# Kernel optimization log

Measured on AMD Instinct MI355X. Metric: run time of the kernel, lower is better.

## Reference

```python
import jax, jax.numpy as jnp
import numpy as np

B, S, D, H = 2, 2048, 1024, 16
HD = D // H


def setup_inputs() -> dict:
    key = jax.random.key(0)
    ks = jax.random.split(key, 12)
    s = 0.02
    inp = {
        "query": jax.random.normal(ks[0], (B, S, D), dtype=jnp.float32),
        "Wq": jax.random.normal(ks[1], (D, D), dtype=jnp.float32) * s,
        "bq": jnp.zeros((D,), jnp.float32),
        "Wk": jax.random.normal(ks[2], (D, D), dtype=jnp.float32) * s,
        "bk": jnp.zeros((D,), jnp.float32),
        "Wv": jax.random.normal(ks[3], (D, D), dtype=jnp.float32) * s,
        "bv": jnp.zeros((D,), jnp.float32),
        "Wo": jax.random.normal(ks[4], (D, D), dtype=jnp.float32) * s,
        "bo": jnp.zeros((D,), jnp.float32),
        "Wm1": jax.random.normal(ks[5], (D // 4, D), dtype=jnp.float32) * s,
        "bm1": jnp.zeros((D // 4,), jnp.float32),
        "Wm2": jax.random.normal(ks[6], (D, D // 4), dtype=jnp.float32) * s,
        "bm2": jnp.zeros((D,), jnp.float32),
        "dopamine": jnp.ones((1,), jnp.float32),
        "serotonin": jnp.ones((1,), jnp.float32),
        "norepinephrine": jnp.ones((1,), jnp.float32),
        "acetylcholine": jnp.ones((1,), jnp.float32),
        "attention_scale": jnp.ones((1,), jnp.float32),
        "attention_bias": jnp.zeros((1,), jnp.float32),
    }
    return inp


def reference(query, Wq, bq, Wk, bk, Wv, bv, Wo, bo, Wm1, bm1, Wm2, bm2,
              dopamine, serotonin, norepinephrine, acetylcholine,
              attention_scale, attention_bias):
    b, s, d = query.shape
    scale = HD ** -0.5
    split = lambda t: t.reshape(b, s, H, HD).transpose(0, 2, 1, 3)  # [b,h,s,hd]
    q = split(query @ Wq.T + bq)
    k = split(query @ Wk.T + bk)
    v = split(query @ Wv.T + bv)
    scores = jnp.einsum('bhqd,bhkd->bhqk', q, k) * scale
    w = jax.nn.softmax(scores, axis=-1)  # dropout=0 (eval)
    attn = jnp.einsum('bhqk,bhkd->bhqd', w, v)
    # neuromodulation MLP on flattened query, then combined scalar gate
    mod = jax.nn.relu(query @ Wm1.T + bm1) @ Wm2.T + bm2  # [b,s,d]
    gate = (dopamine + serotonin + norepinephrine + acetylcholine) / 4.0  # [1]
    neuro = split(mod * gate)  # [b,h,s,hd]
    attn = (attn * attention_scale + attention_bias) * (1.0 + neuro)
    out = attn.transpose(0, 2, 1, 3).reshape(b, s, d) @ Wo.T + bo
    return out
```

## Files before the change

### kernel.cpp

```cpp
#include <hip/hip_runtime.h>
#include <stdint.h>
#include <math.h>


typedef __attribute__((ext_vector_type(8))) short short8;
typedef __attribute__((ext_vector_type(8))) unsigned short ushort8;
typedef __attribute__((ext_vector_type(4))) float floatx4;

#define MFMA16(a, b, c) __builtin_amdgcn_mfma_f32_16x16x32_bf16(a, b, c, 0, 0, 0)

__device__ __forceinline__ unsigned short f2bf(float f) {
    union { float f; uint32_t u; } v; v.f = f;
    uint32_t r = v.u + 0x7fffu + ((v.u >> 16) & 1u);
    return (unsigned short)(r >> 16);
}
__device__ __forceinline__ float bf2f(unsigned short s) {
    union { uint32_t u; float f; } v; v.u = ((uint32_t)s) << 16;
    return v.f;
}

typedef const __attribute__((address_space(1))) void gvoid_t;
typedef __attribute__((address_space(3))) void lvoid_t;
__device__ __forceinline__ void gld16(const void* g, void* l) {
    __builtin_amdgcn_global_load_lds((gvoid_t*)g, (lvoid_t*)l, 16, 0, 0);
}

template<int BN, bool OUTBF>
__device__ __forceinline__ void gemm_core(const unsigned short* __restrict__ A,
                                          const unsigned short* __restrict__ W,
                                          const float* __restrict__ bias,
                                          void* __restrict__ C,
                                          int N, int K, int bm, int bn,
                                          bool relu, float osc)
{
    constexpr int MT = (BN == 128) ? 4 : 2;
    constexpr int SU = (BN == 128) ? 4 : 3;
    __shared__ __align__(16) unsigned short As[128][32];
    __shared__ __align__(16) unsigned short Ws[BN][32];

    const int tid  = threadIdx.x;
    const int w    = tid >> 6, lane = tid & 63;
    const int ln   = lane & 15, quad = lane >> 4;
    const int wm   = (BN == 128) ? (w >> 1) * 64 : w * 32;
    const int wn   = (BN == 128) ? (w & 1) * 64 : 0;

    floatx4 acc[MT][4] = {};

    for (int k0 = 0; k0 < K; k0 += 32) {
        __syncthreads();
        #pragma unroll
        for (int i = 0; i < SU; i++) {
            const int t = w * SU + i;
            if (t < 8) {
                const int r0  = t * 16;
                const int row = r0 + (lane >> 2);
                const int c   = (lane & 3) ^ ((row >> 1) & 3);
                gld16(&A[(size_t)(bm + row) * K + k0 + c * 8], &As[r0][0]);
            } else {
                const int r0  = (t - 8) * 16;
                const int row = r0 + (lane >> 2);
                const int c   = (lane & 3) ^ ((row >> 1) & 3);
                gld16(&W[(size_t)(bn + row) * K + k0 + c * 8], &Ws[r0][0]);
            }
        }
        __syncthreads();

        short8 af[MT], bf[4];
        #pragma unroll
        for (int mt = 0; mt < MT; mt++) {
            const int row = wm + mt * 16 + ln;
            af[mt] = *(const short8*)&As[row][(quad ^ ((row >> 1) & 3)) * 8];
        }
        #pragma unroll
        for (int nt = 0; nt < 4; nt++) {
            const int row = wn + nt * 16 + ln;
            bf[nt] = *(const short8*)&Ws[row][(quad ^ ((row >> 1) & 3)) * 8];
        }
        #pragma unroll
        for (int mt = 0; mt < MT; mt++)
            #pragma unroll
            for (int nt = 0; nt < 4; nt++)
                acc[mt][nt] = MFMA16(af[mt], bf[nt], acc[mt][nt]);
    }

    float bv[4];
    #pragma unroll
    for (int nt = 0; nt < 4; nt++) bv[nt] = bias[bn + wn + nt * 16 + ln];

    #pragma unroll
    for (int mt = 0; mt < MT; mt++) {
        #pragma unroll
        for (int nt = 0; nt < 4; nt++) {
            #pragma unroll
            for (int r = 0; r < 4; r++) {
                float v = (acc[mt][nt][r] + bv[nt]) * osc;
                if (relu) v = fmaxf(v, 0.f);
                const size_t row = (size_t)bm + wm + mt * 16 + quad * 4 + r;
                const size_t col = (size_t)bn + wn + nt * 16 + ln;
                if (OUTBF) ((unsigned short*)C)[row * N + col] = f2bf(v);
                else       ((float*)C)[row * N + col] = v;
            }
        }
    }
}

__global__ __launch_bounds__(256) void qkv_mlp1_gemm(
    const unsigned short* __restrict__ A,
    const unsigned short* __restrict__ Wq, const unsigned short* __restrict__ Wk,
    const unsigned short* __restrict__ Wv, const unsigned short* __restrict__ Wm1,
    const float* __restrict__ bq, const float* __restrict__ bk,
    const float* __restrict__ bv, const float* __restrict__ bm1,
    unsigned short* __restrict__ Qo, unsigned short* __restrict__ Ko,
    unsigned short* __restrict__ Vo, unsigned short* __restrict__ Ho)
{
    const int bx = blockIdx.x, bm = blockIdx.y * 128;
    const unsigned short* W; const float* bias; unsigned short* C;
    int N, bn; bool relu = false; float osc = 1.f;
    if (bx < 8)       { W = Wq;  bias = bq;  C = Qo; N = 1024; bn = bx * 128; osc = 0.125f; }
    else if (bx < 16) { W = Wk;  bias = bk;  C = Ko; N = 1024; bn = (bx - 8) * 128; }
    else if (bx < 24) { W = Wv;  bias = bv;  C = Vo; N = 1024; bn = (bx - 16) * 128; }
    else              { W = Wm1; bias = bm1; C = Ho; N = 256;  bn = (bx - 24) * 128; relu = true; }
    gemm_core<128, true>(A, W, bias, C, N, 1024, bm, bn, relu, osc);
}

template<bool OUTBF>
__global__ __launch_bounds__(256) void gemm_bn64(const unsigned short* __restrict__ A,
                                                 const unsigned short* __restrict__ W,
                                                 const float* __restrict__ bias,
                                                 void* __restrict__ C, int N, int K)
{
    gemm_core<64, OUTBF>(A, W, bias, C, N, K, blockIdx.y * 128, blockIdx.x * 64,
                         false, 1.f);
}

__global__ __launch_bounds__(256) void attn_mfma(const unsigned short* __restrict__ Qg,
                                                 const unsigned short* __restrict__ Kg,
                                                 const unsigned short* __restrict__ Vtg,
                                                 const unsigned short* __restrict__ Modg,
                                                 unsigned short* __restrict__ Yg,
                                                 const float* __restrict__ dop,
                                                 const float* __restrict__ ser,
                                                 const float* __restrict__ nor,
                                                 const float* __restrict__ ach,
                                                 const float* __restrict__ asc,
                                                 const float* __restrict__ abi)
{
    __shared__ __align__(16) unsigned short Ks[128][64];
    __shared__ __align__(16) unsigned short Vs[64][128];
    __shared__ __align__(16) unsigned short Ps[4][2][16][64];

    const int tid = threadIdx.x;
    const int w   = tid >> 6, lane = tid & 63;
    const int ln  = lane & 15, quad = lane >> 4;
    const int qt  = blockIdx.x, h = blockIdx.y, b = blockIdx.z;

    const size_t qrowbase = (size_t)b * 2048 + qt * 128 + w * 32;
    short8 qf[2][2];
    #pragma unroll
    for (int q2 = 0; q2 < 2; q2++) {
        const unsigned short* qp = Qg + (qrowbase + q2 * 16 + ln) * 1024 + h * 64;
        qf[q2][0] = *(const short8*)&qp[quad * 8];
        qf[q2][1] = *(const short8*)&qp[32 + quad * 8];
    }

    const size_t kbase = (size_t)b * 2048 * 1024 + h * 64;
    const size_t vbase = (size_t)(b * 16 + h) * 64 * 2048;

    floatx4 o[2][4] = {};
    float lsum[2] = {0.f, 0.f};

    for (int kc = 0; kc < 16; kc++) {
        __syncthreads();
        #pragma unroll
        for (int i = 0; i < 8; i++) {
            const int t = w * 8 + i;
            if (t < 16) {
                const int R = t * 8 + (lane >> 3);
                const int c = (lane & 7) ^ (R & 7);
                gld16(&Kg[kbase + (size_t)(kc * 128 + R) * 1024 + c * 8], &Ks[t * 8][0]);
            } else {
                const int tv = t - 16;
                const int R  = tv * 4 + (lane >> 4);
                const int c  = (lane & 15) ^ (R & 15);
                gld16(&Vtg[vbase + (size_t)R * 2048 + kc * 128 + c * 8], &Vs[tv * 4][0]);
            }
        }
        __syncthreads();

        #pragma unroll
        for (int half = 0; half < 2; half++) {
            #pragma unroll
            for (int q2 = 0; q2 < 2; q2++) {
                floatx4 sc[4];
                #pragma unroll
                for (int mt = 0; mt < 4; mt++) {
                    const int row = half * 64 + mt * 16 + ln;
                    const short8 kf0 = *(const short8*)&Ks[row][((0 + quad) ^ (ln & 7)) * 8];
                    const short8 kf1 = *(const short8*)&Ks[row][((4 + quad) ^ (ln & 7)) * 8];
                    floatx4 z = {};
                    z = MFMA16(kf0, qf[q2][0], z);
                    z = MFMA16(kf1, qf[q2][1], z);
                    sc[mt] = z;
                }
                #pragma unroll
                for (int mt = 0; mt < 4; mt++) {
                    const float p0 = __expf(sc[mt][0]);
                    const float p1 = __expf(sc[mt][1]);
                    const float p2 = __expf(sc[mt][2]);
                    const float p3 = __expf(sc[mt][3]);
                    lsum[q2] += (p0 + p1) + (p2 + p3);
                    uint2 pk;
                    pk.x = (uint32_t)f2bf(p0) | ((uint32_t)f2bf(p1) << 16);
                    pk.y = (uint32_t)f2bf(p2) | ((uint32_t)f2bf(p3) << 16);
                    const int c2 = (mt * 2 + (quad >> 1)) ^ (ln & 7);
                    *(uint2*)((char*)&Ps[w][q2][ln][0] + c2 * 16 + (quad & 1) * 8) = pk;
                }
            }

            short8 pf[2][2];
            #pragma unroll
            for (int q2 = 0; q2 < 2; q2++)
                #pragma unroll
                for (int ks = 0; ks < 2; ks++) {
                    const int c2 = (ks * 4 + quad) ^ (ln & 7);
                    pf[q2][ks] = *(const short8*)((char*)&Ps[w][q2][ln][0] + c2 * 16);
                }
            #pragma unroll
            for (int ntv = 0; ntv < 4; ntv++) {
                const int vrow = ntv * 16 + ln;
                #pragma unroll
                for (int ks = 0; ks < 2; ks++) {
                    const int c2 = (half * 8 + ks * 4 + quad) ^ (ln & 15);
                    const short8 vf = *(const short8*)&Vs[vrow][c2 * 8];
                    o[0][ntv] = MFMA16(pf[0][ks], vf, o[0][ntv]);
                    o[1][ntv] = MFMA16(pf[1][ks], vf, o[1][ntv]);
                }
            }
        }
    }

    #pragma unroll
    for (int q2 = 0; q2 < 2; q2++) {
        float s = lsum[q2];
        s += __shfl_xor(s, 16);
        s += __shfl_xor(s, 32);
        lsum[q2] = s;
    }

    const float gate = 0.25f * (dop[0] + ser[0] + nor[0] + ach[0]);
    const float scb = asc[0], bib = abi[0];
    #pragma unroll
    for (int q2 = 0; q2 < 2; q2++) {
        #pragma unroll
        for (int r = 0; r < 4; r++) {
            const float inv = 1.f / __shfl(lsum[q2], quad * 4 + r);
            const size_t row = qrowbase + q2 * 16 + quad * 4 + r;
            #pragma unroll
            for (int ntv = 0; ntv < 4; ntv++) {
                const size_t col = (size_t)h * 64 + ntv * 16 + ln;
                const float x  = o[q2][ntv][r] * inv;
                const float mo = bf2f(Modg[row * 1024 + col]);
                const float y  = (x * scb + bib) * (1.f + mo * gate);
                Yg[row * 1024 + col] = f2bf(y);
            }
        }
    }
}

__global__ __launch_bounds__(256) void transpose_v(const unsigned short* __restrict__ Vb,
                                                   unsigned short* __restrict__ Vt)
{
    __shared__ __align__(16) unsigned short T[64][72];
    const int tid = threadIdx.x;
    const int s0 = blockIdx.x * 64, h = blockIdx.y, b = blockIdx.z;
    const int g = tid & 7;
    #pragma unroll
    for (int p = 0; p < 2; p++) {
        const int row = p * 32 + (tid >> 3);
        const ushort8 v = *(const ushort8*)&Vb[(size_t)(b * 2048 + s0 + row) * 1024 + h * 64 + g * 8];
        *(ushort8*)&T[row][g * 8] = v;
    }
    __syncthreads();
    #pragma unroll
    for (int p = 0; p < 2; p++) {
        const int hd = p * 32 + (tid >> 3);
        ushort8 ov;
        #pragma unroll
        for (int j = 0; j < 8; j++) ov[j] = T[g * 8 + j][hd];
        *(ushort8*)&Vt[((size_t)(b * 16 + h) * 64 + hd) * 2048 + s0 + g * 8] = ov;
    }
}

__global__ __launch_bounds__(256) void fused_cast(
    const float* __restrict__ q,   const float* __restrict__ wq,
    const float* __restrict__ wk,  const float* __restrict__ wv,
    const float* __restrict__ wo,  const float* __restrict__ wm1,
    const float* __restrict__ wm2,
    unsigned short* __restrict__ dq,  unsigned short* __restrict__ dwq,
    unsigned short* __restrict__ dwk, unsigned short* __restrict__ dwv,
    unsigned short* __restrict__ dwo, unsigned short* __restrict__ dwm1,
    unsigned short* __restrict__ dwm2)
{
    const size_t u = (size_t)blockIdx.x * 256 + threadIdx.x;
    const float* src; unsigned short* dst; size_t off;
    if      (u <  524288) { src = q;   dst = dq;   off = u; }
    else if (u <  655360) { src = wq;  dst = dwq;  off = u - 524288; }
    else if (u <  786432) { src = wk;  dst = dwk;  off = u - 655360; }
    else if (u <  917504) { src = wv;  dst = dwv;  off = u - 786432; }
    else if (u < 1048576) { src = wo;  dst = dwo;  off = u - 917504; }
    else if (u < 1081344) { src = wm1; dst = dwm1; off = u - 1048576; }
    else                  { src = wm2; dst = dwm2; off = u - 1081344; }
    const float4* p = (const float4*)src + off * 2;
    const float4 a = p[0], c = p[1];
    ushort8 o;
    o[0] = f2bf(a.x); o[1] = f2bf(a.y); o[2] = f2bf(a.z); o[3] = f2bf(a.w);
    o[4] = f2bf(c.x); o[5] = f2bf(c.y); o[6] = f2bf(c.z); o[7] = f2bf(c.w);
    *(ushort8*)&dst[off * 8] = o;
}

extern "C" void kernel_launch(void* const* d_in, const int* in_sizes, int n_in,
                              void* d_out, int out_size, void* d_ws, size_t ws_size,
                              hipStream_t stream)
{
    const float* query = (const float*)d_in[0];
    const float* Wq  = (const float*)d_in[1];
    const float* bq  = (const float*)d_in[2];
    const float* Wk  = (const float*)d_in[3];
    const float* bk  = (const float*)d_in[4];
    const float* Wv  = (const float*)d_in[5];
    const float* bv  = (const float*)d_in[6];
    const float* Wo  = (const float*)d_in[7];
    const float* bo  = (const float*)d_in[8];
    const float* Wm1 = (const float*)d_in[9];
    const float* bm1 = (const float*)d_in[10];
    const float* Wm2 = (const float*)d_in[11];
    const float* bm2 = (const float*)d_in[12];
    const float* dop = (const float*)d_in[13];
    const float* ser = (const float*)d_in[14];
    const float* nor = (const float*)d_in[15];
    const float* ach = (const float*)d_in[16];
    const float* asc = (const float*)d_in[17];
    const float* abi = (const float*)d_in[18];

    char* ws = (char*)d_ws;
    const size_t MB = 1024 * 1024;
    unsigned short* Qry  = (unsigned short*)(ws);
    unsigned short* Wqb  = (unsigned short*)(ws + 8 * MB);
    unsigned short* Wkb  = (unsigned short*)(ws + 10 * MB);
    unsigned short* Wvb  = (unsigned short*)(ws + 12 * MB);
    unsigned short* Wob  = (unsigned short*)(ws + 14 * MB);
    unsigned short* Wm1b = (unsigned short*)(ws + 16 * MB);
    unsigned short* Wm2b = (unsigned short*)(ws + 16 * MB + 512 * 1024);
    unsigned short* Qb   = (unsigned short*)(ws + 17 * MB);
    unsigned short* Kb   = (unsigned short*)(ws + 25 * MB);
    unsigned short* Vb   = (unsigned short*)(ws + 33 * MB);
    unsigned short* Vt   = (unsigned short*)(ws + 41 * MB);
    unsigned short* Yb   = (unsigned short*)(ws + 49 * MB);
    unsigned short* Hm   = (unsigned short*)(ws + 57 * MB);
    unsigned short* Modb = Vb;

    fused_cast<<<4352, 256, 0, stream>>>(query, Wq, Wk, Wv, Wo, Wm1, Wm2,
                                         Qry, Wqb, Wkb, Wvb, Wob, Wm1b, Wm2b);

    qkv_mlp1_gemm<<<dim3(26, 32), 256, 0, stream>>>(
        Qry, Wqb, Wkb, Wvb, Wm1b, bq, bk, bv, bm1, Qb, Kb, Vb, Hm);

    transpose_v<<<dim3(32, 16, 2), 256, 0, stream>>>(Vb, Vt);

    gemm_bn64<true><<<dim3(16, 32), 256, 0, stream>>>(Hm, Wm2b, bm2, (void*)Modb, 1024, 256);

    attn_mfma<<<dim3(16, 16, 2), 256, 0, stream>>>(Qb, Kb, Vt, Modb, Yb,
                                                   dop, ser, nor, ach, asc, abi);

    gemm_bn64<false><<<dim3(16, 32), 256, 0, stream>>>(Yb, Wob, bo, d_out, 1024, 1024);
}
```

Baseline: 255.5 us.

## Fuse V transpose into QKV GEMM epilogue and double-buffer attention K/V tiles

```diff
diff --git a/kernel.cpp b/kernel.cpp
--- a/kernel.cpp
+++ b/kernel.cpp
@@ -1,4 +1,5 @@
 #include <hip/hip_runtime.h>
+#include <hip/hip_bf16.h>
 #include <stdint.h>
 #include <math.h>
 
@@ -17,6 +18,10 @@
 __device__ __forceinline__ float bf2f(unsigned short s) {
     union { uint32_t u; float f; } v; v.u = ((uint32_t)s) << 16;
     return v.f;
+}
+__device__ __forceinline__ uint32_t pk2(float a, float b) {
+    __hip_bfloat162 t = __float22bfloat162_rn(make_float2(a, b));
+    uint32_t u; __builtin_memcpy(&u, &t, 4); return u;
 }
 
 typedef const __attribute__((address_space(1))) void gvoid_t;
@@ -31,7 +36,8 @@
                                           const float* __restrict__ bias,
                                           void* __restrict__ C,
                                           int N, int K, int bm, int bn,
-                                          bool relu, float osc)
+                                          bool relu, float osc,
+                                          unsigned short* __restrict__ vt)
 {
     constexpr int MT = (BN == 128) ? 4 : 2;
     constexpr int SU = (BN == 128) ? 4 : 3;
@@ -87,6 +93,26 @@
     #pragma unroll
     for (int nt = 0; nt < 4; nt++) bv[nt] = bias[bn + wn + nt * 16 + ln];
 
+    if (vt != nullptr) {
+        #pragma unroll
+        for (int mt = 0; mt < MT; mt++) {
+            const int rowg = bm + wm + mt * 16 + quad * 4;
+            const int b = rowg >> 11, s = rowg & 2047;
+            #pragma unroll
+            for (int nt = 0; nt < 4; nt++) {
+                const int n = bn + wn + nt * 16 + ln;
+                const int h = n >> 6, hd = n & 63;
+                float v0 = acc[mt][nt][0] + bv[nt];
+                float v1 = acc[mt][nt][1] + bv[nt];
+                float v2 = acc[mt][nt][2] + bv[nt];
+                float v3 = acc[mt][nt][3] + bv[nt];
+                uint2 pk; pk.x = pk2(v0, v1); pk.y = pk2(v2, v3);
+                *(uint2*)&vt[((size_t)(b * 16 + h) * 64 + hd) * 2048 + s] = pk;
+            }
+        }
+        return;
+    }
+
     #pragma unroll
     for (int mt = 0; mt < MT; mt++) {
         #pragma unroll
@@ -111,16 +137,17 @@
     const float* __restrict__ bq, const float* __restrict__ bk,
     const float* __restrict__ bv, const float* __restrict__ bm1,
     unsigned short* __restrict__ Qo, unsigned short* __restrict__ Ko,
-    unsigned short* __restrict__ Vo, unsigned short* __restrict__ Ho)
+    unsigned short* __restrict__ Vt, unsigned short* __restrict__ Ho)
 {
     const int bx = blockIdx.x, bm = blockIdx.y * 128;
-    const unsigned short* W; const float* bias; unsigned short* C;
+    const unsigned short* W; const float* bias; unsigned short* C = nullptr;
+    unsigned short* vt = nullptr;
     int N, bn; bool relu = false; float osc = 1.f;
     if (bx < 8)       { W = Wq;  bias = bq;  C = Qo; N = 1024; bn = bx * 128; osc = 0.125f; }
     else if (bx < 16) { W = Wk;  bias = bk;  C = Ko; N = 1024; bn = (bx - 8) * 128; }
-    else if (bx < 24) { W = Wv;  bias = bv;  C = Vo; N = 1024; bn = (bx - 16) * 128; }
+    else if (bx < 24) { W = Wv;  bias = bv;  vt = Vt; N = 1024; bn = (bx - 16) * 128; }
     else              { W = Wm1; bias = bm1; C = Ho; N = 256;  bn = (bx - 24) * 128; relu = true; }
-    gemm_core<128, true>(A, W, bias, C, N, 1024, bm, bn, relu, osc);
+    gemm_core<128, true>(A, W, bias, C, N, 1024, bm, bn, relu, osc, vt);
 }
 
 template<bool OUTBF>
@@ -130,7 +157,7 @@
                                                  void* __restrict__ C, int N, int K)
 {
     gemm_core<64, OUTBF>(A, W, bias, C, N, K, blockIdx.y * 128, blockIdx.x * 64,
-                         false, 1.f);
+                         false, 1.f, nullptr);
 }
 
 __global__ __launch_bounds__(256) void attn_mfma(const unsigned short* __restrict__ Qg,
@@ -145,8 +172,8 @@
                                                  const float* __restrict__ asc,
                                                  const float* __restrict__ abi)
 {
-    __shared__ __align__(16) unsigned short Ks[128][64];
-    __shared__ __align__(16) unsigned short Vs[64][128];
+    __shared__ __align__(16) unsigned short Ks[2][128][64];
+    __shared__ __align__(16) unsigned short Vs[2][64][128];
     __shared__ __align__(16) unsigned short Ps[4][2][16][64];
 
     const int tid = threadIdx.x;
@@ -154,6 +181,9 @@
     const int ln  = lane & 15, quad = lane >> 4;
     const int qt  = blockIdx.x, h = blockIdx.y, b = blockIdx.z;
 
+    const size_t kbase = (size_t)b * 2048 * 1024 + h * 64;
+    const size_t vbase = (size_t)(b * 16 + h) * 64 * 2048;
+
     const size_t qrowbase = (size_t)b * 2048 + qt * 128 + w * 32;
     short8 qf[2][2];
     #pragma unroll
@@ -163,43 +193,51 @@
         qf[q2][1] = *(const short8*)&qp[32 + quad * 8];
     }
 
-    const size_t kbase = (size_t)b * 2048 * 1024 + h * 64;
-    const size_t vbase = (size_t)(b * 16 + h) * 64 * 2048;
-
     floatx4 o[2][4] = {};
     float lsum[2] = {0.f, 0.f};
 
-    for (int kc = 0; kc < 16; kc++) {
-        __syncthreads();
+    auto stage = [&](int kc, int bb) {
         #pragma unroll
         for (int i = 0; i < 8; i++) {
             const int t = w * 8 + i;
             if (t < 16) {
                 const int R = t * 8 + (lane >> 3);
                 const int c = (lane & 7) ^ (R & 7);
-                gld16(&Kg[kbase + (size_t)(kc * 128 + R) * 1024 + c * 8], &Ks[t * 8][0]);
+                gld16(&Kg[kbase + (size_t)(kc * 128 + R) * 1024 + c * 8], &Ks[bb][t * 8][0]);
             } else {
                 const int tv = t - 16;
                 const int R  = tv * 4 + (lane >> 4);
                 const int c  = (lane & 15) ^ (R & 15);
-                gld16(&Vtg[vbase + (size_t)R * 2048 + kc * 128 + c * 8], &Vs[tv * 4][0]);
-            }
-        }
+                gld16(&Vtg[vbase + (size_t)R * 2048 + kc * 128 + c * 8], &Vs[bb][tv * 4][0]);
+            }
+        }
+    };
+
+    stage(0, 0);
+
+    for (int kc = 0; kc < 16; kc++) {
+        const int bb = kc & 1;
         __syncthreads();
+        if (kc + 1 < 16) stage(kc + 1, bb ^ 1);
 
         #pragma unroll
         for (int half = 0; half < 2; half++) {
+            short8 kf[4][2];
+            #pragma unroll
+            for (int mt = 0; mt < 4; mt++) {
+                const int row = half * 64 + mt * 16 + ln;
+                kf[mt][0] = *(const short8*)&Ks[bb][row][((0 + quad) ^ (ln & 7)) * 8];
+                kf[mt][1] = *(const short8*)&Ks[bb][row][((4 + quad) ^ (ln & 7)) * 8];
+            }
+
             #pragma unroll
             for (int q2 = 0; q2 < 2; q2++) {
                 floatx4 sc[4];
                 #pragma unroll
                 for (int mt = 0; mt < 4; mt++) {
-                    const int row = half * 64 + mt * 16 + ln;
-                    const short8 kf0 = *(const short8*)&Ks[row][((0 + quad) ^ (ln & 7)) * 8];
-                    const short8 kf1 = *(const short8*)&Ks[row][((4 + quad) ^ (ln & 7)) * 8];
                     floatx4 z = {};
-                    z = MFMA16(kf0, qf[q2][0], z);
-                    z = MFMA16(kf1, qf[q2][1], z);
+                    z = MFMA16(kf[mt][0], qf[q2][0], z);
+                    z = MFMA16(kf[mt][1], qf[q2][1], z);
                     sc[mt] = z;
                 }
                 #pragma unroll
@@ -209,9 +247,7 @@
                     const float p2 = __expf(sc[mt][2]);
                     const float p3 = __expf(sc[mt][3]);
                     lsum[q2] += (p0 + p1) + (p2 + p3);
-                    uint2 pk;
-                    pk.x = (uint32_t)f2bf(p0) | ((uint32_t)f2bf(p1) << 16);
-                    pk.y = (uint32_t)f2bf(p2) | ((uint32_t)f2bf(p3) << 16);
+                    uint2 pk; pk.x = pk2(p0, p1); pk.y = pk2(p2, p3);
                     const int c2 = (mt * 2 + (quad >> 1)) ^ (ln & 7);
                     *(uint2*)((char*)&Ps[w][q2][ln][0] + c2 * 16 + (quad & 1) * 8) = pk;
                 }
@@ -231,7 +267,7 @@
                 #pragma unroll
                 for (int ks = 0; ks < 2; ks++) {
                     const int c2 = (half * 8 + ks * 4 + quad) ^ (ln & 15);
-                    const short8 vf = *(const short8*)&Vs[vrow][c2 * 8];
+                    const short8 vf = *(const short8*)&Vs[bb][vrow][c2 * 8];
                     o[0][ntv] = MFMA16(pf[0][ks], vf, o[0][ntv]);
                     o[1][ntv] = MFMA16(pf[1][ks], vf, o[1][ntv]);
                 }
@@ -264,30 +300,6 @@
                 Yg[row * 1024 + col] = f2bf(y);
             }
         }
-    }
-}
-
-__global__ __launch_bounds__(256) void transpose_v(const unsigned short* __restrict__ Vb,
-                                                   unsigned short* __restrict__ Vt)
-{
-    __shared__ __align__(16) unsigned short T[64][72];
-    const int tid = threadIdx.x;
-    const int s0 = blockIdx.x * 64, h = blockIdx.y, b = blockIdx.z;
-    const int g = tid & 7;
-    #pragma unroll
-    for (int p = 0; p < 2; p++) {
-        const int row = p * 32 + (tid >> 3);
-        const ushort8 v = *(const ushort8*)&Vb[(size_t)(b * 2048 + s0 + row) * 1024 + h * 64 + g * 8];
-        *(ushort8*)&T[row][g * 8] = v;
-    }
-    __syncthreads();
-    #pragma unroll
-    for (int p = 0; p < 2; p++) {
-        const int hd = p * 32 + (tid >> 3);
-        ushort8 ov;
-        #pragma unroll
-        for (int j = 0; j < 8; j++) ov[j] = T[g * 8 + j][hd];
-        *(ushort8*)&Vt[((size_t)(b * 16 + h) * 64 + hd) * 2048 + s0 + g * 8] = ov;
     }
 }
 
@@ -312,10 +324,10 @@
     else                  { src = wm2; dst = dwm2; off = u - 1081344; }
     const float4* p = (const float4*)src + off * 2;
     const float4 a = p[0], c = p[1];
-    ushort8 o;
-    o[0] = f2bf(a.x); o[1] = f2bf(a.y); o[2] = f2bf(a.z); o[3] = f2bf(a.w);
-    o[4] = f2bf(c.x); o[5] = f2bf(c.y); o[6] = f2bf(c.z); o[7] = f2bf(c.w);
-    *(ushort8*)&dst[off * 8] = o;
+    uint4 o;
+    o.x = pk2(a.x, a.y); o.y = pk2(a.z, a.w);
+    o.z = pk2(c.x, c.y); o.w = pk2(c.z, c.w);
+    *(uint4*)&dst[off * 8] = o;
 }
 
 extern "C" void kernel_launch(void* const* d_in, const int* in_sizes, int n_in,
@@ -353,19 +365,16 @@
     unsigned short* Wm2b = (unsigned short*)(ws + 16 * MB + 512 * 1024);
     unsigned short* Qb   = (unsigned short*)(ws + 17 * MB);
     unsigned short* Kb   = (unsigned short*)(ws + 25 * MB);
-    unsigned short* Vb   = (unsigned short*)(ws + 33 * MB);
+    unsigned short* Modb = (unsigned short*)(ws + 33 * MB);
     unsigned short* Vt   = (unsigned short*)(ws + 41 * MB);
     unsigned short* Yb   = (unsigned short*)(ws + 49 * MB);
     unsigned short* Hm   = (unsigned short*)(ws + 57 * MB);
-    unsigned short* Modb = Vb;
 
     fused_cast<<<4352, 256, 0, stream>>>(query, Wq, Wk, Wv, Wo, Wm1, Wm2,
                                          Qry, Wqb, Wkb, Wvb, Wob, Wm1b, Wm2b);
 
     qkv_mlp1_gemm<<<dim3(26, 32), 256, 0, stream>>>(
-        Qry, Wqb, Wkb, Wvb, Wm1b, bq, bk, bv, bm1, Qb, Kb, Vb, Hm);
-
-    transpose_v<<<dim3(32, 16, 2), 256, 0, stream>>>(Vb, Vt);
+        Qry, Wqb, Wkb, Wvb, Wm1b, bq, bk, bv, bm1, Qb, Kb, Vt, Hm);
 
     gemm_bn64<true><<<dim3(16, 32), 256, 0, stream>>>(Hm, Wm2b, bm2, (void*)Modb, 1024, 256);
 
```

New measurement: 242.3 us. 1.05x faster.
